# Kernel optimization log

Hardware: AMD Instinct MI355X
Metric: run time of the kernel (lower is better)

## Reference

```python
import jax, jax.numpy as jnp
import numpy as np

B, C1, C2, H, W = 8, 256, 256, 64, 64
C = 256            # int(c1*e)
G = C // 16        # 16 groups (dg)
Cg = C // G        # 16 channels per group
K = 9              # 3x3 kernel sample points
BN_EPS = 1e-5

# kernel grid offsets for 3x3, dilation 1 (pad=1 centers the grid)
KH = jnp.array([-1, -1, -1, 0, 0, 0, 1, 1, 1], jnp.float32)
KW = jnp.array([-1, 0, 1, -1, 0, 1, -1, 0, 1], jnp.float32)


def setup_inputs() -> dict:
    key = jax.random.key(0)
    ks = jax.random.split(key, 10)
    x = jax.random.normal(ks[0], (B, C1, H, W), jnp.float32)
    w_cv1 = jax.random.normal(ks[1], (C, C1), jnp.float32) / np.sqrt(C1)
    b_cv1 = jax.random.normal(ks[2], (C,), jnp.float32) * 0.1
    # offset/mask linear (DCNv4 inits to zero; small scale keeps sampling sane)
    w_off = jax.random.normal(ks[3], (G * 3 * K, C), jnp.float32) * 0.01
    b_off = jax.random.normal(ks[4], (G * 3 * K,), jnp.float32) * 0.01
    w_cv2 = jax.random.normal(ks[5], (C2, C), jnp.float32) / np.sqrt(C)
    bn_gamma = jax.random.uniform(ks[6], (C2,), jnp.float32, 0.5, 1.5)
    bn_beta = jax.random.normal(ks[7], (C2,), jnp.float32) * 0.1
    bn_mean = jax.random.normal(ks[8], (C2,), jnp.float32) * 0.1
    bn_var = jax.random.uniform(ks[9], (C2,), jnp.float32, 0.5, 1.5)
    return dict(x=x, w_cv1=w_cv1, b_cv1=b_cv1, w_off=w_off, b_off=b_off,
                w_cv2=w_cv2, bn_gamma=bn_gamma, bn_beta=bn_beta,
                bn_mean=bn_mean, bn_var=bn_var)


def _gather(vflat, hi, wi):
    # vflat: (B, H*W, G, Cg); hi/wi: (B,H,W,K,G) float corner indices
    ok = ((hi >= 0) & (hi < H) & (wi >= 0) & (wi < W)).astype(vflat.dtype)
    idx = (jnp.clip(hi, 0, H - 1) * W + jnp.clip(wi, 0, W - 1)).astype(jnp.int32)
    idx = idx.reshape(B, H * W * K, G)
    idxb = jnp.broadcast_to(idx[..., None], (B, H * W * K, G, Cg))
    g = jnp.take_along_axis(vflat, idxb, axis=1)  # (B, HWK, G, Cg)
    return g.reshape(B, H, W, K, G, Cg), ok


def _dcnv4(v, off, mask):
    # v: (B,H,W,G,Cg); off: (B,H,W,G,K,2) (dh,dw); mask: (B,H,W,G,K)
    ii = jnp.arange(H, dtype=jnp.float32)
    jj = jnp.arange(W, dtype=jnp.float32)
    ph = ii[None, :, None, None, None] + KH[None, None, None, None, :] + off[..., 0]
    pw = jj[None, None, :, None, None] + KW[None, None, None, None, :] + off[..., 1]
    ph = ph.transpose(0, 1, 2, 4, 3)  # (B,H,W,K,G)
    pw = pw.transpose(0, 1, 2, 4, 3)
    h0 = jnp.floor(ph); w0 = jnp.floor(pw)
    ah = ph - h0; aw = pw - w0
    vflat = v.reshape(B, H * W, G, Cg)
    g00, ok00 = _gather(vflat, h0, w0)
    g01, ok01 = _gather(vflat, h0, w0 + 1)
    g10, ok10 = _gather(vflat, h0 + 1, w0)
    g11, ok11 = _gather(vflat, h0 + 1, w0 + 1)
    w00 = ((1 - ah) * (1 - aw) * ok00)[..., None]
    w01 = ((1 - ah) * aw * ok01)[..., None]
    w10 = (ah * (1 - aw) * ok10)[..., None]
    w11 = (ah * aw * ok11)[..., None]
    sample = w00 * g00 + w01 * g01 + w10 * g10 + w11 * g11  # (B,H,W,K,G,Cg)
    out = jnp.einsum('bhwkgc,bhwgk->bhwgc', sample, mask)
    return out.reshape(B, H, W, C).transpose(0, 3, 1, 2)  # NCHW


def reference(x, w_cv1, b_cv1, w_off, b_off, w_cv2, bn_gamma, bn_beta, bn_mean, bn_var):
    # cv1: 1x1 conv
    h1 = jnp.einsum('bchw,oc->bohw', x, w_cv1) + b_cv1[None, :, None, None]
    # offset/mask 1x1 projection, per-group layout [2K offsets, K masks]
    om = jnp.einsum('bchw,oc->bhwo', h1, w_off) + b_off
    om = om.reshape(B, H, W, G, 3 * K)
    off = om[..., :2 * K].reshape(B, H, W, G, K, 2)
    mask = om[..., 2 * K:]  # DCNv4: no softmax, used directly
    v = h1.transpose(0, 2, 3, 1).reshape(B, H, W, G, Cg)
    y = _dcnv4(v, off, mask)
    # cv2: 1x1 conv (no bias)
    y = jnp.einsum('bchw,oc->bohw', y, w_cv2)
    # BatchNorm (eval mode)
    scale = (bn_gamma / jnp.sqrt(bn_var + BN_EPS))[None, :, None, None]
    y = (y - bn_mean[None, :, None, None]) * scale + bn_beta[None, :, None, None]
    # SiLU
    return y * jax.nn.sigmoid(y)
```

## Files before the change

kernel.cpp:

```cpp
#include <hip/hip_runtime.h>

#define HW 4096
#define CCH 256
#define MOFF 432
#define PTOT 32768
#define PDIM 68
#define PIMG (PDIM*PDIM)

typedef unsigned short u16;
typedef __attribute__((ext_vector_type(8))) short short8;
typedef __attribute__((ext_vector_type(8))) unsigned short u16x8;
typedef __attribute__((ext_vector_type(4))) unsigned short u16x4;
typedef __attribute__((ext_vector_type(4))) float f32x4;

__device__ __forceinline__ u16 f2b(float f){
  unsigned int u = __float_as_uint(f);
  unsigned int rounding = 0x7FFFu + ((u >> 16) & 1u);
  return (u16)((u + rounding) >> 16);
}
__device__ __forceinline__ float b2f(u16 s){
  return __uint_as_float(((unsigned int)s) << 16);
}

__global__ __launch_bounds__(256) void k_prep(const float* __restrict__ x,
    const float* __restrict__ w1, const float* __restrict__ w2,
    const float* __restrict__ woff, const float* __restrict__ b1,
    const float* __restrict__ boff,
    const float* __restrict__ gamma, const float* __restrict__ beta,
    const float* __restrict__ mean, const float* __restrict__ var,
    u16* __restrict__ xT, u16* __restrict__ wb_big, u16* __restrict__ wb2,
    float* __restrict__ bnA, float* __restrict__ bnB,
    float* __restrict__ bcomb, u16* __restrict__ h1p){
  __shared__ float tile[64][65];
  const int r = blockIdx.x, t = threadIdx.x;
  if (r < 2048){
    const int pb = (r & 63) * 64, cb = ((r >> 6) & 3) * 64, b = r >> 8;
    const float* src = x + ((size_t)(b * CCH + cb)) * HW + pb;
    #pragma unroll
    for (int pass = 0; pass < 4; ++pass){
      int c_l = pass * 16 + (t >> 4);
      int pq = (t & 15) * 4;
      float4 v = *reinterpret_cast<const float4*>(&src[(size_t)c_l * HW + pq]);
      tile[pq + 0][c_l] = v.x; tile[pq + 1][c_l] = v.y;
      tile[pq + 2][c_l] = v.z; tile[pq + 3][c_l] = v.w;
    }
    __syncthreads();
    #pragma unroll
    for (int pass = 0; pass < 4; ++pass){
      int p_l = pass * 16 + (t >> 4);
      int cq = (t & 15) * 4;
      u16x4 o4;
      #pragma unroll
      for (int j = 0; j < 4; ++j) o4[j] = f2b(tile[p_l][cq + j]);
      *reinterpret_cast<u16x4*>(&xT[((size_t)b * HW + pb + p_l) * CCH + cb + cq]) = o4;
    }
  }
  else if (r < 2304){ int o = r - 2048; wb_big[o*256 + t] = f2b(w1[o*256 + t]); }
  else if (r < 2384){ wb_big[(688 + (r - 2304)) * 256 + t] = 0; }
  else if (r < 2640){ int o = r - 2384; wb2[o*256 + t] = f2b(w2[o*256 + t]); }
  else if (r == 2640){
    if (t < 256){
      float sc = gamma[t] * rsqrtf(var[t] + 1e-5f);
      bnA[t] = sc;
      bnB[t] = beta[t] - mean[t] * sc;
    }
  } else if (r < 3169){
    int n = (r - 2641) * 128 + (t >> 1);
    int seg = t & 1;
    int plane = n / 528, m = n % 528;
    int row, col;
    if (m < 136){ row = m / 68; col = m % 68; }
    else if (m < 272){ int mm = m - 136; row = 66 + mm / 68; col = mm % 68; }
    else { int mm = m - 272; row = 2 + (mm >> 2); int c4 = mm & 3; col = (c4 & 1) + 66 * (c4 >> 1); }
    u16x8 z = {};
    *reinterpret_cast<u16x8*>(&h1p[((size_t)plane * PIMG + row * PDIM + col) * 16 + seg * 8]) = z;
  } else {
    float* wr_ = &tile[0][0];
    float* pb  = wr_ + 256;
    const int j = r - 3169;
    wr_[t] = woff[j * 256 + t];
    __syncthreads();
    float s = 0.f;
    #pragma unroll 8
    for (int m = 0; m < 256; ++m) s += wr_[m] * w1[m * 256 + t];
    wb_big[(256 + j) * 256 + t] = f2b(s);
    pb[t] = wr_[t] * b1[t];
    __syncthreads();
    if (t == 0){
      float bs = boff[j];
      for (int m = 0; m < 256; ++m) bs += pb[m];
      bcomb[j] = bs;
    }
  }
}

__global__ __launch_bounds__(256, 2) void k_gemm_big(const u16* __restrict__ A,
    const u16* __restrict__ Bw, const float* __restrict__ b1,
    const float* __restrict__ bcomb, u16* __restrict__ h1p,
    u16* __restrict__ om){
  __shared__ __align__(16) u16 smem[34816];
  u16* As = smem;
  u16* Bs = smem + 256 * 72;

  const int bid = blockIdx.x;
  const int xcd = bid & 7, s = bid >> 3;
  const int row_local = s / 6, cblk = s % 6;
  const int tm = (row_local * 8 + xcd) * 256;
  const int tn = cblk * 128;

  const int t = threadIdx.x;
  const int lane = t & 63;
  const int wid = t >> 6;
  const int wr = wid >> 1, wc = wid & 1;

  f32x4 acc[8][4] = {};

  for (int kc = 0; kc < 256; kc += 64){
    #pragma unroll
    for (int i = 0; i < 8; ++i){
      int idx = t + i * 256;
      int row = idx >> 3, cq = idx & 7;
      *reinterpret_cast<u16x8*>(&As[row * 72 + cq * 8]) =
        *reinterpret_cast<const u16x8*>(&A[(size_t)(tm + row) * 256 + kc + cq * 8]);
    }
    #pragma unroll
    for (int i = 0; i < 4; ++i){
      int idx = t + i * 256;
      int row = idx >> 3, cq = idx & 7;
      *reinterpret_cast<u16x8*>(&Bs[row * 72 + cq * 8]) =
        *reinterpret_cast<const u16x8*>(&Bw[(size_t)(tn + row) * 256 + kc + cq * 8]);
    }
    __syncthreads();
    #pragma unroll
    for (int kk = 0; kk < 2; ++kk){
      short8 af[8], bf[4];
      #pragma unroll
      for (int m = 0; m < 8; ++m)
        af[m] = *reinterpret_cast<const short8*>(
          &As[(wr * 128 + m * 16 + (lane & 15)) * 72 + kk * 32 + (lane >> 4) * 8]);
      #pragma unroll
      for (int n = 0; n < 4; ++n)
        bf[n] = *reinterpret_cast<const short8*>(
          &Bs[(wc * 64 + n * 16 + (lane & 15)) * 72 + kk * 32 + (lane >> 4) * 8]);
      #pragma unroll
      for (int m = 0; m < 8; ++m)
        #pragma unroll
        for (int n = 0; n < 4; ++n)
          acc[m][n] = __builtin_amdgcn_mfma_f32_16x16x32_bf16(af[m], bf[n], acc[m][n], 0, 0, 0);
    }
    __syncthreads();
  }

  constexpr int CP = 136;
  u16* C_l = smem;
  #pragma unroll
  for (int n = 0; n < 4; ++n){
    int col = wc * 64 + n * 16 + (lane & 15);
    int o = tn + col;
    float bi = (o < 256) ? b1[o] : ((o - 256 < MOFF) ? bcomb[o - 256] : 0.f);
    #pragma unroll
    for (int m = 0; m < 8; ++m){
      int r0 = wr * 128 + m * 16 + ((lane >> 4) << 2);
      #pragma unroll
      for (int j = 0; j < 4; ++j)
        C_l[(r0 + j) * CP + col] = f2b(acc[m][n][j] + bi);
    }
  }
  __syncthreads();
  #pragma unroll
  for (int pass = 0; pass < 16; ++pass){
    int row = pass * 16 + (t >> 4);
    int sg = t & 15;
    int oc = tn + sg * 8;
    int p = tm + row;
    if (tn < 256){
      int bb = p >> 12, ii = (p >> 6) & 63, jj = p & 63;
      size_t dst = ((size_t)(bb * 16 + (oc >> 4)) * PIMG + (ii + 2) * PDIM + jj + 2) * 16 + (oc & 15);
      *reinterpret_cast<u16x8*>(&h1p[dst]) =
        *reinterpret_cast<const u16x8*>(&C_l[row * CP + sg * 8]);
    } else {
      int occ = oc - 256;
      if (occ + 8 <= MOFF)
        *reinterpret_cast<u16x8*>(&om[(size_t)p * MOFF + occ]) =
          *reinterpret_cast<const u16x8*>(&C_l[row * CP + sg * 8]);
    }
  }
}

__global__ __launch_bounds__(256) void k_gemm2(const u16* __restrict__ A,
    const u16* __restrict__ Bw, const float* __restrict__ bnA,
    const float* __restrict__ bnB, float* __restrict__ out){
  __shared__ __align__(16) u16 smem[(128 + 128) * 40];
  const int t = threadIdx.x;
  const int tm = blockIdx.x * 128;
  const int tn = blockIdx.y * 128;
  const int lane = t & 63;
  const int wid = t >> 6;
  const int wr = wid >> 1, wc = wid & 1;
  constexpr int BOFF = 128 * 40;

  f32x4 acc[4][4] = {};

  for (int kc = 0; kc < 256; kc += 32){
    #pragma unroll
    for (int i = 0; i < 2; ++i){
      int v = t + i * 256;
      int row = v >> 2, cq = v & 3;
      *reinterpret_cast<u16x8*>(&smem[row * 40 + cq * 8]) =
        *reinterpret_cast<const u16x8*>(&A[(size_t)(tm + row) * 256 + kc + cq * 8]);
    }
    #pragma unroll
    for (int i = 0; i < 2; ++i){
      int v = t + i * 256;
      int row = v >> 2, cq = v & 3;
      *reinterpret_cast<u16x8*>(&smem[BOFF + row * 40 + cq * 8]) =
        *reinterpret_cast<const u16x8*>(&Bw[(size_t)(tn + row) * 256 + kc + cq * 8]);
    }
    __syncthreads();
    short8 af[4], bf[4];
    #pragma unroll
    for (int m = 0; m < 4; ++m)
      af[m] = *reinterpret_cast<const short8*>(
        &smem[(wr * 64 + m * 16 + (lane & 15)) * 40 + (lane >> 4) * 8]);
    #pragma unroll
    for (int n = 0; n < 4; ++n)
      bf[n] = *reinterpret_cast<const short8*>(
        &smem[BOFF + (wc * 64 + n * 16 + (lane & 15)) * 40 + (lane >> 4) * 8]);
    #pragma unroll
    for (int m = 0; m < 4; ++m)
      #pragma unroll
      for (int n = 0; n < 4; ++n)
        acc[m][n] = __builtin_amdgcn_mfma_f32_16x16x32_bf16(af[m], bf[n], acc[m][n], 0, 0, 0);
    __syncthreads();
  }

  const int bimg = tm >> 12;
  const int ploc = tm & 4095;
  #pragma unroll
  for (int n = 0; n < 4; ++n){
    int o = tn + wc * 64 + n * 16 + (lane & 15);
    float sA = bnA[o], sB = bnB[o];
    #pragma unroll
    for (int m = 0; m < 4; ++m){
      int prow = wr * 64 + m * 16 + ((lane >> 4) << 2);
      f32x4 st;
      #pragma unroll
      for (int j = 0; j < 4; ++j){
        float y = acc[m][n][j] * sA + sB;
        st[j] = y / (1.f + expf(-y));
      }
      *reinterpret_cast<f32x4*>(&out[((size_t)(bimg * 256 + o)) * HW + ploc + prow]) = st;
    }
  }
}

__global__ __launch_bounds__(256) void k_sample(const u16* __restrict__ h1p,
    const u16* __restrict__ om, u16* __restrict__ ydcn){
  __shared__ float oms[4 * MOFF];
  const int t = threadIdx.x;
  const int pblk = blockIdx.x * 4;
  if (t < 216){
    u16x8 v = *reinterpret_cast<const u16x8*>(&om[(size_t)pblk * MOFF + t * 8]);
    float4 lo, hi;
    lo.x = b2f(v[0]); lo.y = b2f(v[1]); lo.z = b2f(v[2]); lo.w = b2f(v[3]);
    hi.x = b2f(v[4]); hi.y = b2f(v[5]); hi.z = b2f(v[6]); hi.w = b2f(v[7]);
    *reinterpret_cast<float4*>(&oms[t * 8]) = lo;
    *reinterpret_cast<float4*>(&oms[t * 8 + 4]) = hi;
  }
  __syncthreads();

  const int px = t >> 6;
  const int g = (t >> 2) & 15;
  const int q = t & 3;
  const int p = pblk + px;
  const int b = p >> 12, hw = p & 4095;
  const int ic = hw >> 6, jc = hw & 63;
  const u16* plane = h1p + (size_t)(b * 16 + g) * PIMG * 16;
  const float* ob = &oms[px * MOFF + g * 27];
  const float fi = (float)ic, fj = (float)jc;
  const bool wsel = (q >= 2);

  float acc[8] = {};
  #pragma unroll
  for (int k = 0; k < 9; ++k){
    float oh = ob[2 * k], ow = ob[2 * k + 1], m = ob[18 + k];
    float ph = fi + (float)(k / 3 - 1) + oh;
    float pw = fj + (float)(k % 3 - 1) + ow;
    float h0f = floorf(ph), w0f = floorf(pw);
    float ah = ph - h0f, aw = pw - w0f;
    int h0 = (int)h0f, w0 = (int)w0f;
    int hc = min(max(h0, -2), 64) + 2;
    int wc = min(max(w0, -2), 64) + 2;
    const u16* cbase = plane + ((hc * PDIM + wc) << 4) + (q << 3);
    u16x8 tv = *reinterpret_cast<const u16x8*>(cbase);
    u16x8 bv = *reinterpret_cast<const u16x8*>(cbase + PDIM * 16);
    float mh1 = m * ah, mh0 = m - mh1;
    float awq = wsel ? aw : (1.f - aw);
    float ct = mh0 * awq, cb = mh1 * awq;
    #pragma unroll
    for (int j = 0; j < 8; ++j)
      acc[j] += ct * b2f(tv[j]) + cb * b2f(bv[j]);
  }
  #pragma unroll
  for (int j = 0; j < 8; ++j)
    acc[j] += __shfl_xor(acc[j], 2, 64);
  if (q < 2){
    u16x8 o8;
    #pragma unroll
    for (int j = 0; j < 8; ++j) o8[j] = f2b(acc[j]);
    *reinterpret_cast<u16x8*>(&ydcn[(size_t)p * 256 + g * 16 + q * 8]) = o8;
  }
}

extern "C" void kernel_launch(void* const* d_in, const int* in_sizes, int n_in,
                              void* d_out, int out_size, void* d_ws, size_t ws_size,
                              hipStream_t stream) {
  const float* x     = (const float*)d_in[0];
  const float* w1    = (const float*)d_in[1];
  const float* b1    = (const float*)d_in[2];
  const float* woff  = (const float*)d_in[3];
  const float* boff  = (const float*)d_in[4];
  const float* w2    = (const float*)d_in[5];
  const float* gamma = (const float*)d_in[6];
  const float* beta  = (const float*)d_in[7];
  const float* mean  = (const float*)d_in[8];
  const float* var   = (const float*)d_in[9];
  float* out = (float*)d_out;
  (void)in_sizes; (void)n_in; (void)out_size; (void)ws_size;

  u16* h1p    = (u16*)d_ws;
  u16* om     = h1p + (size_t)128 * PIMG * 16;
  u16* xT     = om + (size_t)PTOT * MOFF;
  u16* ydcn   = xT + (size_t)PTOT * CCH;
  u16* wb_big = ydcn + (size_t)PTOT * CCH;
  u16* wb2    = wb_big + 768 * 256;
  float* bnA  = (float*)(wb2 + 256 * 256);
  float* bnB  = bnA + 256;
  float* bcomb = bnB + 256;

  dim3 blk(256);
  k_prep<<<dim3(3601), blk, 0, stream>>>(x, w1, w2, woff, b1, boff,
                                         gamma, beta, mean, var,
                                         xT, wb_big, wb2, bnA, bnB, bcomb, h1p);
  k_gemm_big<<<dim3(768), blk, 0, stream>>>(xT, wb_big, b1, bcomb, h1p, om);
  k_sample<<<dim3(PTOT / 4), blk, 0, stream>>>(h1p, om, ydcn);
  k_gemm2<<<dim3(PTOT / 128, 2), blk, 0, stream>>>(ydcn, wb2, bnA, bnB, out);
}
```

Measured before the change: 103.1 us.

## Fuse deformable sampling into cv2 GEMM with BN+SiLU epilogue via LDS

Merges the sampling kernel and the second GEMM into one 512-thread kernel. Each block samples 64 pixels into an LDS A-tile, then multiplies it by all 256 output channels and applies BN and SiLU. This removes the global write and re-read of the bf16 ydcn intermediate and one kernel launch. In exchange, the weight tile is reloaded by every block, there is a sync after each 8-pixel sampling chunk, and the GEMM tiles are smaller, which may lower MFMA efficiency and occupancy.

```diff
diff --git a/kernel.cpp b/kernel.cpp
--- a/kernel.cpp
+++ b/kernel.cpp
@@ -187,128 +187,128 @@
   }
 }
 
-__global__ __launch_bounds__(256) void k_gemm2(const u16* __restrict__ A,
-    const u16* __restrict__ Bw, const float* __restrict__ bnA,
-    const float* __restrict__ bnB, float* __restrict__ out){
-  __shared__ __align__(16) u16 smem[(128 + 128) * 40];
+__global__ __launch_bounds__(512, 4) void k_fuse(const u16* __restrict__ h1p,
+    const u16* __restrict__ om, const u16* __restrict__ Bw,
+    const float* __restrict__ bnA, const float* __restrict__ bnB,
+    float* __restrict__ out){
+  __shared__ __align__(16) u16 A_lds[64 * 264];
+  __shared__ __align__(16) u16 scratch[10240];
+  float* oms = (float*)scratch;
+  u16* Bs = scratch;
+
   const int t = threadIdx.x;
-  const int tm = blockIdx.x * 128;
-  const int tn = blockIdx.y * 128;
+  const int tm = blockIdx.x * 64;
+  const int b = tm >> 12;
+
+  const int px8 = t >> 6;
+  const int g = (t >> 2) & 15;
+  const int q = t & 3;
+  const int xsel = q >> 1;
+  const u16* plane = h1p + (size_t)(b * 16 + g) * PIMG * 16;
+
+  for (int c8 = 0; c8 < 8; ++c8){
+    {
+      const u16* src = om + (size_t)(tm + c8 * 8) * MOFF;
+      if (t < 432){
+        u16x8 v = *reinterpret_cast<const u16x8*>(&src[t * 8]);
+        float4 lo, hi;
+        lo.x = b2f(v[0]); lo.y = b2f(v[1]); lo.z = b2f(v[2]); lo.w = b2f(v[3]);
+        hi.x = b2f(v[4]); hi.y = b2f(v[5]); hi.z = b2f(v[6]); hi.w = b2f(v[7]);
+        *reinterpret_cast<float4*>(&oms[t * 8]) = lo;
+        *reinterpret_cast<float4*>(&oms[t * 8 + 4]) = hi;
+      }
+    }
+    __syncthreads();
+
+    const int lpx = c8 * 8 + px8;
+    const int p = tm + lpx;
+    const int hw = p & 4095;
+    const int ic = hw >> 6, jc = hw & 63;
+    const float* ob = &oms[px8 * MOFF + g * 27];
+    const float fi = (float)ic, fj = (float)jc;
+    const u16* lanebase = plane + q * 8;
+
+    float acc[8] = {};
+    #pragma unroll
+    for (int k = 0; k < 9; ++k){
+      float oh = ob[2 * k], ow = ob[2 * k + 1], m = ob[18 + k];
+      float ph = fi + (float)(k / 3 - 1) + oh;
+      float pw = fj + (float)(k % 3 - 1) + ow;
+      float h0f = floorf(ph), w0f = floorf(pw);
+      float ah = ph - h0f, aw = pw - w0f;
+      int h0 = (int)h0f, w0 = (int)w0f;
+      int hc = min(max(h0, -2), 64) + 2;
+      int wc = min(max(w0, -2), 64) + 2;
+      const u16* c0 = lanebase + ((hc * PDIM + wc) << 4);
+      u16x8 tv = *reinterpret_cast<const u16x8*>(c0);
+      u16x8 bv = *reinterpret_cast<const u16x8*>(c0 + PDIM * 16);
+      float mh1 = m * ah, mh0 = m - mh1;
+      float awq = xsel ? aw : (1.f - aw);
+      float ct = mh0 * awq, cb = mh1 * awq;
+      #pragma unroll
+      for (int j = 0; j < 8; ++j)
+        acc[j] += ct * b2f(tv[j]) + cb * b2f(bv[j]);
+    }
+    #pragma unroll
+    for (int j = 0; j < 8; ++j)
+      acc[j] += __shfl_xor(acc[j], 2, 64);
+    if (q < 2){
+      u16x8 o8;
+      #pragma unroll
+      for (int j = 0; j < 8; ++j) o8[j] = f2b(acc[j]);
+      *reinterpret_cast<u16x8*>(&A_lds[lpx * 264 + g * 16 + q * 8]) = o8;
+    }
+    __syncthreads();
+  }
+
   const int lane = t & 63;
   const int wid = t >> 6;
-  const int wr = wid >> 1, wc = wid & 1;
-  constexpr int BOFF = 128 * 40;
-
-  f32x4 acc[4][4] = {};
+  const int wr = wid >> 2, wc = wid & 3;
+
+  f32x4 gacc[2][4] = {};
 
   for (int kc = 0; kc < 256; kc += 32){
     #pragma unroll
     for (int i = 0; i < 2; ++i){
-      int v = t + i * 256;
-      int row = v >> 2, cq = v & 3;
-      *reinterpret_cast<u16x8*>(&smem[row * 40 + cq * 8]) =
-        *reinterpret_cast<const u16x8*>(&A[(size_t)(tm + row) * 256 + kc + cq * 8]);
-    }
-    #pragma unroll
-    for (int i = 0; i < 2; ++i){
-      int v = t + i * 256;
-      int row = v >> 2, cq = v & 3;
-      *reinterpret_cast<u16x8*>(&smem[BOFF + row * 40 + cq * 8]) =
-        *reinterpret_cast<const u16x8*>(&Bw[(size_t)(tn + row) * 256 + kc + cq * 8]);
-    }
-    __syncthreads();
-    short8 af[4], bf[4];
-    #pragma unroll
-    for (int m = 0; m < 4; ++m)
+      int idx = t + i * 512;
+      int row = idx >> 2, cq = idx & 3;
+      *reinterpret_cast<u16x8*>(&Bs[row * 40 + cq * 8]) =
+        *reinterpret_cast<const u16x8*>(&Bw[(size_t)row * 256 + kc + cq * 8]);
+    }
+    __syncthreads();
+    short8 af[2], bf[4];
+    #pragma unroll
+    for (int m = 0; m < 2; ++m)
       af[m] = *reinterpret_cast<const short8*>(
-        &smem[(wr * 64 + m * 16 + (lane & 15)) * 40 + (lane >> 4) * 8]);
+        &A_lds[(wr * 32 + m * 16 + (lane & 15)) * 264 + kc + (lane >> 4) * 8]);
     #pragma unroll
     for (int n = 0; n < 4; ++n)
       bf[n] = *reinterpret_cast<const short8*>(
-        &smem[BOFF + (wc * 64 + n * 16 + (lane & 15)) * 40 + (lane >> 4) * 8]);
-    #pragma unroll
-    for (int m = 0; m < 4; ++m)
+        &Bs[(wc * 64 + n * 16 + (lane & 15)) * 40 + (lane >> 4) * 8]);
+    #pragma unroll
+    for (int m = 0; m < 2; ++m)
       #pragma unroll
       for (int n = 0; n < 4; ++n)
-        acc[m][n] = __builtin_amdgcn_mfma_f32_16x16x32_bf16(af[m], bf[n], acc[m][n], 0, 0, 0);
-    __syncthreads();
-  }
-
-  const int bimg = tm >> 12;
+        gacc[m][n] = __builtin_amdgcn_mfma_f32_16x16x32_bf16(af[m], bf[n], gacc[m][n], 0, 0, 0);
+    __syncthreads();
+  }
+
   const int ploc = tm & 4095;
   #pragma unroll
   for (int n = 0; n < 4; ++n){
-    int o = tn + wc * 64 + n * 16 + (lane & 15);
+    int o = wc * 64 + n * 16 + (lane & 15);
     float sA = bnA[o], sB = bnB[o];
     #pragma unroll
-    for (int m = 0; m < 4; ++m){
-      int prow = wr * 64 + m * 16 + ((lane >> 4) << 2);
+    for (int m = 0; m < 2; ++m){
+      int prow = wr * 32 + m * 16 + ((lane >> 4) << 2);
       f32x4 st;
       #pragma unroll
       for (int j = 0; j < 4; ++j){
-        float y = acc[m][n][j] * sA + sB;
+        float y = gacc[m][n][j] * sA + sB;
         st[j] = y / (1.f + expf(-y));
       }
-      *reinterpret_cast<f32x4*>(&out[((size_t)(bimg * 256 + o)) * HW + ploc + prow]) = st;
-    }
-  }
-}
-
-__global__ __launch_bounds__(256) void k_sample(const u16* __restrict__ h1p,
-    const u16* __restrict__ om, u16* __restrict__ ydcn){
-  __shared__ float oms[4 * MOFF];
-  const int t = threadIdx.x;
-  const int pblk = blockIdx.x * 4;
-  if (t < 216){
-    u16x8 v = *reinterpret_cast<const u16x8*>(&om[(size_t)pblk * MOFF + t * 8]);
-    float4 lo, hi;
-    lo.x = b2f(v[0]); lo.y = b2f(v[1]); lo.z = b2f(v[2]); lo.w = b2f(v[3]);
-    hi.x = b2f(v[4]); hi.y = b2f(v[5]); hi.z = b2f(v[6]); hi.w = b2f(v[7]);
-    *reinterpret_cast<float4*>(&oms[t * 8]) = lo;
-    *reinterpret_cast<float4*>(&oms[t * 8 + 4]) = hi;
-  }
-  __syncthreads();
-
-  const int px = t >> 6;
-  const int g = (t >> 2) & 15;
-  const int q = t & 3;
-  const int p = pblk + px;
-  const int b = p >> 12, hw = p & 4095;
-  const int ic = hw >> 6, jc = hw & 63;
-  const u16* plane = h1p + (size_t)(b * 16 + g) * PIMG * 16;
-  const float* ob = &oms[px * MOFF + g * 27];
-  const float fi = (float)ic, fj = (float)jc;
-  const bool wsel = (q >= 2);
-
-  float acc[8] = {};
-  #pragma unroll
-  for (int k = 0; k < 9; ++k){
-    float oh = ob[2 * k], ow = ob[2 * k + 1], m = ob[18 + k];
-    float ph = fi + (float)(k / 3 - 1) + oh;
-    float pw = fj + (float)(k % 3 - 1) + ow;
-    float h0f = floorf(ph), w0f = floorf(pw);
-    float ah = ph - h0f, aw = pw - w0f;
-    int h0 = (int)h0f, w0 = (int)w0f;
-    int hc = min(max(h0, -2), 64) + 2;
-    int wc = min(max(w0, -2), 64) + 2;
-    const u16* cbase = plane + ((hc * PDIM + wc) << 4) + (q << 3);
-    u16x8 tv = *reinterpret_cast<const u16x8*>(cbase);
-    u16x8 bv = *reinterpret_cast<const u16x8*>(cbase + PDIM * 16);
-    float mh1 = m * ah, mh0 = m - mh1;
-    float awq = wsel ? aw : (1.f - aw);
-    float ct = mh0 * awq, cb = mh1 * awq;
-    #pragma unroll
-    for (int j = 0; j < 8; ++j)
-      acc[j] += ct * b2f(tv[j]) + cb * b2f(bv[j]);
-  }
-  #pragma unroll
-  for (int j = 0; j < 8; ++j)
-    acc[j] += __shfl_xor(acc[j], 2, 64);
-  if (q < 2){
-    u16x8 o8;
-    #pragma unroll
-    for (int j = 0; j < 8; ++j) o8[j] = f2b(acc[j]);
-    *reinterpret_cast<u16x8*>(&ydcn[(size_t)p * 256 + g * 16 + q * 8]) = o8;
+      *reinterpret_cast<f32x4*>(&out[((size_t)(b * 256 + o)) * HW + ploc + prow]) = st;
+    }
   }
 }
 
@@ -331,8 +331,7 @@
   u16* h1p    = (u16*)d_ws;
   u16* om     = h1p + (size_t)128 * PIMG * 16;
   u16* xT     = om + (size_t)PTOT * MOFF;
-  u16* ydcn   = xT + (size_t)PTOT * CCH;
-  u16* wb_big = ydcn + (size_t)PTOT * CCH;
+  u16* wb_big = xT + (size_t)PTOT * CCH;
   u16* wb2    = wb_big + 768 * 256;
   float* bnA  = (float*)(wb2 + 256 * 256);
   float* bnB  = bnA + 256;
@@ -343,6 +342,5 @@
                                          gamma, beta, mean, var,
                                          xT, wb_big, wb2, bnA, bnB, bcomb, h1p);
   k_gemm_big<<<dim3(768), blk, 0, stream>>>(xT, wb_big, b1, bcomb, h1p, om);
-  k_sample<<<dim3(PTOT / 4), blk, 0, stream>>>(h1p, om, ydcn);
-  k_gemm2<<<dim3(PTOT / 128, 2), blk, 0, stream>>>(ydcn, wb2, bnA, bnB, out);
-}
+  k_fuse<<<dim3(PTOT / 64), dim3(512), 0, stream>>>(h1p, om, wb2, bnA, bnB, out);
+}
```

Result: slower. 106.0 us (+2.8%).
